# Kernel optimization log

Hardware: AMD Instinct MI355X
Metric: run time of the kernel (lower is better)

## Reference

```python
import jax, jax.numpy as jnp
import numpy as np
import math

NUM_BUCKETS = 32
MAX_DISTANCE = 128
N_HEADS = 16
D_KV = 64


def _relative_position_bucket(relative_position, num_buckets=NUM_BUCKETS, max_distance=MAX_DISTANCE):
    # bidirectional (encoder) variant: is_decoder=False
    nb = num_buckets // 2
    rel_buckets = (relative_position > 0).astype(jnp.int32) * nb
    rp = jnp.abs(relative_position)
    max_exact = nb // 2
    is_small = rp < max_exact
    rp_large = max_exact + (
        jnp.log(rp.astype(jnp.float32) / max_exact)
        / math.log(max_distance / max_exact)
        * (nb - max_exact)
    ).astype(jnp.int32)
    rp_large = jnp.minimum(rp_large, nb - 1)
    return rel_buckets + jnp.where(is_small, rp, rp_large)


def compute_position_bias(rel_bias_table, q_len, k_len):
    ctx = jnp.arange(q_len, dtype=jnp.int32)[:, None]
    mem = jnp.arange(k_len, dtype=jnp.int32)[None, :]
    buckets = _relative_position_bucket(mem - ctx)  # [q_len, k_len]
    values = rel_bias_table[buckets]                # [q_len, k_len, H]
    return jnp.transpose(values, (2, 0, 1))[None]   # [1, H, q_len, k_len]


def setup_inputs() -> dict:
    key = jax.random.key(0)
    ks = jax.random.split(key, 6)
    B, S, D = 2, 2048, 1024
    s = 0.02
    return {
        "hidden_states": jax.random.normal(ks[0], (B, S, D), dtype=jnp.float32),
        "Wq": jax.random.normal(ks[1], (D, N_HEADS * D_KV), dtype=jnp.float32) * s,
        "Wk": jax.random.normal(ks[2], (D, N_HEADS * D_KV), dtype=jnp.float32) * s,
        "Wv": jax.random.normal(ks[3], (D, N_HEADS * D_KV), dtype=jnp.float32) * s,
        "Wo": jax.random.normal(ks[4], (N_HEADS * D_KV, D), dtype=jnp.float32) * s,
        "rel_bias_table": jax.random.normal(ks[5], (NUM_BUCKETS, N_HEADS), dtype=jnp.float32),
    }


def reference(hidden_states, Wq, Wk, Wv, Wo, rel_bias_table):
    B, S, D = hidden_states.shape
    H, dh = N_HEADS, D_KV
    q = (hidden_states @ Wq).reshape(B, S, H, dh)
    k = (hidden_states @ Wk).reshape(B, S, H, dh)
    v = (hidden_states @ Wv).reshape(B, S, H, dh)

    position_bias = compute_position_bias(rel_bias_table, S, S)  # [1,H,S,S]

    scale = 1.0 / math.sqrt(dh)  # applied inside optimized_attention (SDPA convention)
    scores = jnp.einsum('bqhd,bkhd->bhqk', q, k) * scale + position_bias
    probs = jax.nn.softmax(scores, axis=-1)
    ctx = jnp.einsum('bhqk,bkhd->bqhd', probs, v).reshape(B, S, H * dh)
    attn_output = ctx @ Wo
    return attn_output
```

## Files before the change

kernel.cpp:

```cpp
#include <hip/hip_runtime.h>

typedef __attribute__((ext_vector_type(8))) short s16x8;
typedef __attribute__((ext_vector_type(4))) float f32x4;
typedef __attribute__((ext_vector_type(4))) unsigned int u32x4;
typedef __attribute__((ext_vector_type(2))) unsigned int u32x2;
typedef unsigned short u16;
typedef unsigned int u32;

#define LOG2E 1.4426950408889634f

__device__ __forceinline__ u16 f2bf(float x) {
  u32 u = __float_as_uint(x);
  u += 0x7FFFu + ((u >> 16) & 1u);
  return (u16)(u >> 16);
}

__device__ __forceinline__ u32 pack_bf_trunc(float lo, float hi) {
  return (__float_as_uint(lo) >> 16) | (__float_as_uint(hi) & 0xFFFF0000u);
}

__device__ __forceinline__ void gl_lds16(const void* g, void* l) {
  __builtin_amdgcn_global_load_lds((const __attribute__((address_space(1))) void*)g,
                                   (__attribute__((address_space(3))) void*)l, 16, 0, 0);
}

#define MFMA16(a, b, c) __builtin_amdgcn_mfma_f32_16x16x32_bf16((a), (b), (c), 0, 0, 0)


__global__ __launch_bounds__(256) void prep(const float* __restrict__ hs,
                                            const float* __restrict__ Wq,
                                            const float* __restrict__ Wk,
                                            const float* __restrict__ Wv,
                                            const float* __restrict__ Wo,
                                            const float* __restrict__ tbl,
                                            u16* __restrict__ hsb,
                                            u16* __restrict__ wt,
                                            u16* __restrict__ wot,
                                            float* __restrict__ biasT) {
  const int blk = blockIdx.x;
  const int tid = threadIdx.x;
  if (blk < 2048) {
    const int i = blk * 256 + tid;
    const float4* s4 = (const float4*)hs;
    float4 a = s4[i * 2];
    float4 b = s4[i * 2 + 1];
    s16x8 o;
    o[0] = (short)f2bf(a.x); o[1] = (short)f2bf(a.y);
    o[2] = (short)f2bf(a.z); o[3] = (short)f2bf(a.w);
    o[4] = (short)f2bf(b.x); o[5] = (short)f2bf(b.y);
    o[6] = (short)f2bf(b.z); o[7] = (short)f2bf(b.w);
    *(s16x8*)&hsb[i * 8] = o;
  } else if (blk < 4096) {
    int r = blk - 2048;
    const int sel = r >> 9;
    r &= 511;
    const float* W = sel == 0 ? Wq : (sel == 1 ? Wk : (sel == 2 ? Wv : Wo));
    u16* dst = sel == 3 ? wot : wt + sel * 1048576;
    const int n = (r & 15) * 64 + (tid & 63);
    const int kb = (r >> 4) * 32 + (tid >> 6) * 8;
    s16x8 o;
#pragma unroll
    for (int j = 0; j < 8; ++j) o[j] = (short)f2bf(W[(kb + j) * 1024 + n]);
    *(s16x8*)&dst[n * 1024 + kb] = o;
  } else {
    const int i = (blk - 4096) * 256 + tid;
    const int h = i >> 12, dp = i & 4095;
    const int delta = dp - 2047;
    const int rp = delta < 0 ? -delta : delta;
    int bucket = delta > 0 ? 16 : 0;
    if (rp < 8)
      bucket += rp;
    else
      bucket += 8 + (rp >= 12) + (rp >= 16) + (rp >= 23) + (rp >= 32) +
                (rp >= 46) + (rp >= 64) + (rp >= 91);
    biasT[i] = tbl[bucket * 16 + h] * LOG2E;
  }
}

__global__ __launch_bounds__(256) void vtrans(const u16* __restrict__ V,
                                              u16* __restrict__ VT) {
  const int tid = threadIdx.x;
  const int bh = blockIdx.y;
  const int b = bh >> 4, h = bh & 15;
  const int s0 = blockIdx.x * 32;
  const int d = tid & 63;
  const int si = tid >> 6;
  s16x8 o;
#pragma unroll
  for (int j = 0; j < 8; ++j)
    o[j] = (short)V[(b * 2048 + s0 + si * 8 + j) * 1024 + h * 64 + d];
  *(s16x8*)&VT[(bh * 64 + d) * 2048 + s0 + si * 8] = o;
}


__device__ __forceinline__ void gemm_core(const u16* __restrict__ A,
                                          const u16* __restrict__ Bt,
                                          int m0, int n0,
                                          u16* As, u16* Bs, f32x4 acc[4][4]) {
  const int tid = threadIdx.x;
  const int w = tid >> 6, l = tid & 63, g = l >> 4, m15 = l & 15;
  const int wr = (w >> 1) * 64, wc = (w & 1) * 64;
#pragma unroll
  for (int i = 0; i < 4; ++i)
#pragma unroll
    for (int j = 0; j < 4; ++j) acc[i][j] = (f32x4){0.f, 0.f, 0.f, 0.f};

  for (int kt = 0; kt < 16; ++kt) {
    const int k0 = kt * 64;
    __syncthreads();
#pragma unroll
    for (int c = 0; c < 4; ++c) {
      const int idx = c * 256 + tid;
      const int row = idx >> 3, col16 = idx & 7;
      const int scol = col16 ^ (row & 7);
      gl_lds16(&A[(m0 + row) * 1024 + k0 + scol * 8], (char*)As + c * 4096 + w * 1024);
      gl_lds16(&Bt[(n0 + row) * 1024 + k0 + scol * 8], (char*)Bs + c * 4096 + w * 1024);
    }
    __syncthreads();
#pragma unroll
    for (int ks = 0; ks < 2; ++ks) {
      s16x8 af[4], bf[4];
#pragma unroll
      for (int mf = 0; mf < 4; ++mf) {
        const int row = wr + mf * 16 + m15;
        af[mf] = *(const s16x8*)&As[(row * 8 + ((ks * 4 + g) ^ (row & 7))) * 8];
      }
#pragma unroll
      for (int nf = 0; nf < 4; ++nf) {
        const int row = wc + nf * 16 + m15;
        bf[nf] = *(const s16x8*)&Bs[(row * 8 + ((ks * 4 + g) ^ (row & 7))) * 8];
      }
#pragma unroll
      for (int mf = 0; mf < 4; ++mf)
#pragma unroll
        for (int nf = 0; nf < 4; ++nf)
          acc[mf][nf] = MFMA16(af[mf], bf[nf], acc[mf][nf]);
    }
  }
}

__global__ __launch_bounds__(256) void gemm_qkv(const u16* __restrict__ X,
                                                const u16* __restrict__ Wt,
                                                u16* __restrict__ Q,
                                                u16* __restrict__ Kb,
                                                u16* __restrict__ Vb) {
  __shared__ u16 As[8192], Bs[8192];
  f32x4 acc[4][4];
  const int flat = blockIdx.x;
  const int x = flat & 7, i = flat >> 3;
  const int m0 = ((x & 3) * 8 + (i & 7)) * 128;
  const int n0 = ((x >> 2) * 12 + (i >> 3)) * 128;
  gemm_core(X, Wt, m0, n0, As, Bs, acc);

  const int tid = threadIdx.x;
  const int w = tid >> 6, l = tid & 63, g = l >> 4, m15 = l & 15;
  const int wr = (w >> 1) * 64, wc = (w & 1) * 64;
  const int nsel = n0 >> 10;
  u16* dst = nsel == 0 ? Q : (nsel == 1 ? Kb : Vb);
  const float scale = nsel == 0 ? 0.125f * LOG2E : 1.0f;
  const int ncol0 = (n0 & 1023) + wc;
#pragma unroll
  for (int mf = 0; mf < 4; ++mf) {
    const int rbase = m0 + wr + mf * 16 + g * 4;
#pragma unroll
    for (int nf = 0; nf < 4; ++nf) {
      const int col = ncol0 + nf * 16 + m15;
#pragma unroll
      for (int r = 0; r < 4; ++r)
        dst[(rbase + r) * 1024 + col] = f2bf(acc[mf][nf][r] * scale);
    }
  }
}

__global__ __launch_bounds__(256) void gemm_out(const u16* __restrict__ CTX,
                                                const u16* __restrict__ Wot,
                                                float* __restrict__ Out) {
  __shared__ u16 As[8192], Bs[8192];
  f32x4 acc[4][4];
  const int flat = blockIdx.x;
  const int x = flat & 7, i = flat >> 3;
  const int m0 = ((x & 3) * 8 + (i & 7)) * 128;
  const int n0 = ((x >> 2) * 4 + (i >> 3)) * 128;
  gemm_core(CTX, Wot, m0, n0, As, Bs, acc);

  const int tid = threadIdx.x;
  const int w = tid >> 6, l = tid & 63, g = l >> 4, m15 = l & 15;
  const int wr = (w >> 1) * 64, wc = (w & 1) * 64;
#pragma unroll
  for (int mf = 0; mf < 4; ++mf) {
    const int rbase = m0 + wr + mf * 16 + g * 4;
#pragma unroll
    for (int nf = 0; nf < 4; ++nf) {
      const int col = n0 + wc + nf * 16 + m15;
#pragma unroll
      for (int r = 0; r < 4; ++r)
        Out[(rbase + r) * 1024 + col] = acc[mf][nf][r];
    }
  }
}


__global__ __launch_bounds__(256, 2) void attn_kernel(const u16* __restrict__ Qg,
                                                      const u16* __restrict__ Kg,
                                                      const u16* __restrict__ VTg,
                                                      const float* __restrict__ biasT,
                                                      const float* __restrict__ tbl,
                                                      u16* __restrict__ CTX) {
  __shared__ u16 KT[2][4096];
  __shared__ u16 VTs[2][4096];

  const int tid = threadIdx.x;
  const int w = tid >> 6, l = tid & 63, g = l >> 4, m15 = l & 15;
  const int flat = blockIdx.x;
  const int nf_ = (flat & 7) * 64 + (flat >> 3);
  const int qblk = nf_ & 15, bh = nf_ >> 4;
  const int b = bh >> 4, h = bh & 15;
  const int qw = qblk * 128 + w * 32;

  const float fpos = tbl[31 * 16 + h] * LOG2E;
  const float fneg = tbl[15 * 16 + h] * LOG2E;

  s16x8 aq[2][2];
#pragma unroll
  for (int qs = 0; qs < 2; ++qs) {
    const u16* qp = &Qg[(b * 2048 + qw + qs * 16 + m15) * 1024 + h * 64 + g * 8];
    aq[qs][0] = *(const s16x8*)qp;
    aq[qs][1] = *(const s16x8*)(qp + 32);
  }

  s16x8 vone;
#pragma unroll
  for (int j = 0; j < 8; ++j) vone[j] = (short)0x3F80;

  f32x4 o[2][4];
  f32x4 ls4[2];
#pragma unroll
  for (int qs = 0; qs < 2; ++qs) {
    ls4[qs] = (f32x4){0.f, 0.f, 0.f, 0.f};
#pragma unroll
    for (int d = 0; d < 4; ++d) o[qs][d] = (f32x4){0.f, 0.f, 0.f, 0.f};
  }

  const u16* Kbase = &Kg[(b * 2048) * 1024 + h * 64];
  const u16* Vbase = &VTg[bh * 64 * 2048];

#define STAGE(buf, kv0)                                                          \
  {                                                                              \
    _Pragma("unroll") for (int c = 0; c < 2; ++c) {                              \
      const int idx = c * 256 + tid;                                             \
      const int row = idx >> 3, col16 = idx & 7;                                 \
      const int scol = col16 ^ (row & 7);                                        \
      gl_lds16(&Kbase[(kv0 + row) * 1024 + scol * 8],                            \
               (char*)KT + (buf)*8192 + c * 4096 + w * 1024);                    \
      gl_lds16(&Vbase[row * 2048 + (kv0) + scol * 8],                            \
               (char*)VTs + (buf)*8192 + c * 4096 + w * 1024);                   \
    }                                                                            \
  }

  STAGE(0, 0);
  int cur = 0;
  for (int t = 0; t < 32; ++t) {
    const int kv0 = t * 64;
    __syncthreads();
    if (t < 31) STAGE(cur ^ 1, kv0 + 64);

    const u16* KTc = &KT[cur][0];
    const u16* VTc = &VTs[cur][0];

    f32x4 s[2][4];
    const int diff = kv0 - qw;
    if (diff <= -160 || diff >= 128) {
      const float bc = diff > 0 ? fpos : fneg;
#pragma unroll
      for (int qs = 0; qs < 2; ++qs)
#pragma unroll
        for (int c = 0; c < 4; ++c) s[qs][c] = (f32x4){bc, bc, bc, bc};
    } else {
#pragma unroll
      for (int qs = 0; qs < 2; ++qs) {
        const float* bp = &biasT[h * 4096 + kv0 + g * 4 - qw - qs * 16 - m15 + 2047];
#pragma unroll
        for (int c = 0; c < 4; ++c)
#pragma unroll
          for (int r = 0; r < 4; ++r) s[qs][c][r] = bp[c * 16 + r];
      }
    }

#pragma unroll
    for (int ks = 0; ks < 2; ++ks) {
#pragma unroll
      for (int c = 0; c < 4; ++c) {
        const int row = c * 16 + m15;
        const s16x8 bk = *(const s16x8*)&KTc[(row * 8 + ((ks * 4 + g) ^ (row & 7))) * 8];
        s[0][c] = MFMA16(bk, aq[0][ks], s[0][c]);
        s[1][c] = MFMA16(bk, aq[1][ks], s[1][c]);
      }
    }

    s16x8 pa[2][2];
#pragma unroll
    for (int qs = 0; qs < 2; ++qs) {
      u32 w01[4], w23[4];
#pragma unroll
      for (int c = 0; c < 4; ++c) {
        w01[c] = pack_bf_trunc(__builtin_amdgcn_exp2f(s[qs][c][0]),
                               __builtin_amdgcn_exp2f(s[qs][c][1]));
        w23[c] = pack_bf_trunc(__builtin_amdgcn_exp2f(s[qs][c][2]),
                               __builtin_amdgcn_exp2f(s[qs][c][3]));
      }
#pragma unroll
      for (int ks = 0; ks < 2; ++ks) {
        u32x2 rA = __builtin_amdgcn_permlane32_swap(w01[2 * ks], w01[2 * ks + 1], false, false);
        u32x2 rB = __builtin_amdgcn_permlane16_swap(rA[0], rA[1], false, false);
        u32x2 rC = __builtin_amdgcn_permlane32_swap(w23[2 * ks], w23[2 * ks + 1], false, false);
        u32x2 rD = __builtin_amdgcn_permlane16_swap(rC[0], rC[1], false, false);
        const u32x4 pd = (u32x4){rB[0], rD[0], rB[1], rD[1]};
        pa[qs][ks] = __builtin_bit_cast(s16x8, pd);
      }
    }

#pragma unroll
    for (int ks = 0; ks < 2; ++ks) {
#pragma unroll
      for (int d = 0; d < 4; ++d) {
        const int rowv = d * 16 + m15;
        const s16x8 bv = *(const s16x8*)&VTc[(rowv * 8 + ((ks * 4 + g) ^ (rowv & 7))) * 8];
        o[0][d] = MFMA16(pa[0][ks], bv, o[0][d]);
        o[1][d] = MFMA16(pa[1][ks], bv, o[1][d]);
      }
      ls4[0] = MFMA16(pa[0][ks], vone, ls4[0]);
      ls4[1] = MFMA16(pa[1][ks], vone, ls4[1]);
    }
    cur ^= 1;
  }
#undef STAGE

#pragma unroll
  for (int qs = 0; qs < 2; ++qs) {
    f32x4 inv;
#pragma unroll
    for (int r = 0; r < 4; ++r) inv[r] = 1.0f / ls4[qs][r];
    const int orow = b * 2048 + qw + qs * 16 + g * 4;
    const int ocol = h * 64 + m15;
#pragma unroll
    for (int d = 0; d < 4; ++d) {
#pragma unroll
      for (int r = 0; r < 4; ++r)
        CTX[(orow + r) * 1024 + ocol + d * 16] = f2bf(o[qs][d][r] * inv[r]);
    }
  }
}


extern "C" void kernel_launch(void* const* d_in, const int* in_sizes, int n_in,
                              void* d_out, int out_size, void* d_ws, size_t ws_size,
                              hipStream_t stream) {
  (void)in_sizes; (void)n_in; (void)out_size; (void)ws_size;
  const float* hs  = (const float*)d_in[0];
  const float* Wq  = (const float*)d_in[1];
  const float* Wk  = (const float*)d_in[2];
  const float* Wv  = (const float*)d_in[3];
  const float* Wo  = (const float*)d_in[4];
  const float* tbl = (const float*)d_in[5];

  char* ws = (char*)d_ws;
  u16* hsb   = (u16*)(ws);
  u16* wt    = (u16*)(ws + 8388608);
  u16* wot   = (u16*)(ws + 14680064);
  u16* q     = (u16*)(ws + 16777216);
  u16* k     = (u16*)(ws + 25165824);
  u16* v     = (u16*)(ws + 33554432);
  u16* vt    = (u16*)(ws + 41943040);
  u16* ctx   = (u16*)(ws + 50331648);
  float* biasT = (float*)(ws + 58720256);

  prep<<<4352, 256, 0, stream>>>(hs, Wq, Wk, Wv, Wo, tbl, hsb, wt, wot, biasT);
  gemm_qkv<<<768, 256, 0, stream>>>(hsb, wt, q, k, v);
  vtrans<<<dim3(64, 32), 256, 0, stream>>>(v, vt);
  attn_kernel<<<512, 256, 0, stream>>>(q, k, vt, biasT, tbl, ctx);
  gemm_out<<<256, 256, 0, stream>>>(ctx, wot, (float*)d_out);
}
```

Baseline: 125.8 us.

## Split attention KV range in two, fuse V transpose into QKV GEMM, add merge

The attention kernel now splits each head's key range into two halves, launching twice as many blocks with occupancy raised to 4 waves per SIMD, and writes unnormalized partial outputs plus row sums. A new merge kernel adds the two halves and normalizes. Because softmax here has no max subtraction, the partials combine without rescaling. The V transpose kernel is removed: the QKV GEMM epilogue writes V directly in transposed layout. s_setprio brackets are added around the MFMA sections. The cost is an extra merge pass, extra partial-output traffic, and bf16 rounding of the partial sums.

Result: slower. 129.3 us (+2.8%).

```diff
diff --git a/kernel.cpp b/kernel.cpp
--- a/kernel.cpp
+++ b/kernel.cpp
@@ -1,6 +1,7 @@
 #include <hip/hip_runtime.h>
 
 typedef __attribute__((ext_vector_type(8))) short s16x8;
+typedef __attribute__((ext_vector_type(4))) short s16x4;
 typedef __attribute__((ext_vector_type(4))) float f32x4;
 typedef __attribute__((ext_vector_type(4))) unsigned int u32x4;
 typedef __attribute__((ext_vector_type(2))) unsigned int u32x2;
@@ -13,6 +14,10 @@
   u32 u = __float_as_uint(x);
   u += 0x7FFFu + ((u >> 16) & 1u);
   return (u16)(u >> 16);
+}
+
+__device__ __forceinline__ float bf2f(u16 x) {
+  return __uint_as_float((u32)x << 16);
 }
 
 __device__ __forceinline__ u32 pack_bf_trunc(float lo, float hi) {
@@ -77,21 +82,6 @@
   }
 }
 
-__global__ __launch_bounds__(256) void vtrans(const u16* __restrict__ V,
-                                              u16* __restrict__ VT) {
-  const int tid = threadIdx.x;
-  const int bh = blockIdx.y;
-  const int b = bh >> 4, h = bh & 15;
-  const int s0 = blockIdx.x * 32;
-  const int d = tid & 63;
-  const int si = tid >> 6;
-  s16x8 o;
-#pragma unroll
-  for (int j = 0; j < 8; ++j)
-    o[j] = (short)V[(b * 2048 + s0 + si * 8 + j) * 1024 + h * 64 + d];
-  *(s16x8*)&VT[(bh * 64 + d) * 2048 + s0 + si * 8] = o;
-}
-
 
 __device__ __forceinline__ void gemm_core(const u16* __restrict__ A,
                                           const u16* __restrict__ Bt,
@@ -143,7 +133,7 @@
                                                 const u16* __restrict__ Wt,
                                                 u16* __restrict__ Q,
                                                 u16* __restrict__ Kb,
-                                                u16* __restrict__ Vb) {
+                                                u16* __restrict__ VT) {
   __shared__ u16 As[8192], Bs[8192];
   f32x4 acc[4][4];
   const int flat = blockIdx.x;
@@ -156,18 +146,35 @@
   const int w = tid >> 6, l = tid & 63, g = l >> 4, m15 = l & 15;
   const int wr = (w >> 1) * 64, wc = (w & 1) * 64;
   const int nsel = n0 >> 10;
-  u16* dst = nsel == 0 ? Q : (nsel == 1 ? Kb : Vb);
-  const float scale = nsel == 0 ? 0.125f * LOG2E : 1.0f;
   const int ncol0 = (n0 & 1023) + wc;
-#pragma unroll
-  for (int mf = 0; mf < 4; ++mf) {
-    const int rbase = m0 + wr + mf * 16 + g * 4;
-#pragma unroll
-    for (int nf = 0; nf < 4; ++nf) {
-      const int col = ncol0 + nf * 16 + m15;
-#pragma unroll
-      for (int r = 0; r < 4; ++r)
-        dst[(rbase + r) * 1024 + col] = f2bf(acc[mf][nf][r] * scale);
+  if (nsel == 2) {
+#pragma unroll
+    for (int mf = 0; mf < 4; ++mf) {
+      const int rbase = m0 + wr + mf * 16 + g * 4;
+      const int bhb = (rbase >> 11) * 16;
+      const int rloc = rbase & 2047;
+#pragma unroll
+      for (int nf = 0; nf < 4; ++nf) {
+        const int col = ncol0 + nf * 16 + m15;
+        s16x4 pk;
+#pragma unroll
+        for (int r = 0; r < 4; ++r) pk[r] = (short)f2bf(acc[mf][nf][r]);
+        *(s16x4*)&VT[((bhb + (col >> 6)) * 64 + (col & 63)) * 2048 + rloc] = pk;
+      }
+    }
+  } else {
+    u16* dst = nsel == 0 ? Q : Kb;
+    const float scale = nsel == 0 ? 0.125f * LOG2E : 1.0f;
+#pragma unroll
+    for (int mf = 0; mf < 4; ++mf) {
+      const int rbase = m0 + wr + mf * 16 + g * 4;
+#pragma unroll
+      for (int nf = 0; nf < 4; ++nf) {
+        const int col = ncol0 + nf * 16 + m15;
+#pragma unroll
+        for (int r = 0; r < 4; ++r)
+          dst[(rbase + r) * 1024 + col] = f2bf(acc[mf][nf][r] * scale);
+      }
     }
   }
 }
@@ -200,22 +207,30 @@
 }
 
 
-__global__ __launch_bounds__(256, 2) void attn_kernel(const u16* __restrict__ Qg,
+__global__ __launch_bounds__(256, 4) void attn_kernel(const u16* __restrict__ Qg,
                                                       const u16* __restrict__ Kg,
                                                       const u16* __restrict__ VTg,
                                                       const float* __restrict__ biasT,
                                                       const float* __restrict__ tbl,
-                                                      u16* __restrict__ CTX) {
+                                                      u16* __restrict__ po0,
+                                                      u16* __restrict__ po1,
+                                                      float* __restrict__ pls) {
   __shared__ u16 KT[2][4096];
   __shared__ u16 VTs[2][4096];
 
   const int tid = threadIdx.x;
   const int w = tid >> 6, l = tid & 63, g = l >> 4, m15 = l & 15;
   const int flat = blockIdx.x;
-  const int nf_ = (flat & 7) * 64 + (flat >> 3);
-  const int qblk = nf_ & 15, bh = nf_ >> 4;
+  const int nf_ = (flat & 7) * 128 + (flat >> 3);
+  const int bh = nf_ >> 5;
+  const int rem = nf_ & 31;
+  const int half = rem >> 4, qblk = rem & 15;
   const int b = bh >> 4, h = bh & 15;
   const int qw = qblk * 128 + w * 32;
+  const int kvbase = half * 1024;
+
+  u16* poh = half ? po1 : po0;
+  float* plsh = pls + half * 65536;
 
   const float fpos = tbl[31 * 16 + h] * LOG2E;
   const float fneg = tbl[15 * 16 + h] * LOG2E;
@@ -241,8 +256,8 @@
     for (int d = 0; d < 4; ++d) o[qs][d] = (f32x4){0.f, 0.f, 0.f, 0.f};
   }
 
-  const u16* Kbase = &Kg[(b * 2048) * 1024 + h * 64];
-  const u16* Vbase = &VTg[bh * 64 * 2048];
+  const u16* Kbase = &Kg[(b * 2048 + kvbase) * 1024 + h * 64];
+  const u16* Vbase = &VTg[bh * 64 * 2048 + kvbase];
 
 #define STAGE(buf, kv0)                                                          \
   {                                                                              \
@@ -259,16 +274,16 @@
 
   STAGE(0, 0);
   int cur = 0;
-  for (int t = 0; t < 32; ++t) {
+  for (int t = 0; t < 16; ++t) {
     const int kv0 = t * 64;
     __syncthreads();
-    if (t < 31) STAGE(cur ^ 1, kv0 + 64);
+    if (t < 15) STAGE(cur ^ 1, kv0 + 64);
 
     const u16* KTc = &KT[cur][0];
     const u16* VTc = &VTs[cur][0];
 
     f32x4 s[2][4];
-    const int diff = kv0 - qw;
+    const int diff = kvbase + kv0 - qw;
     if (diff <= -160 || diff >= 128) {
       const float bc = diff > 0 ? fpos : fneg;
 #pragma unroll
@@ -278,7 +293,8 @@
     } else {
 #pragma unroll
       for (int qs = 0; qs < 2; ++qs) {
-        const float* bp = &biasT[h * 4096 + kv0 + g * 4 - qw - qs * 16 - m15 + 2047];
+        const float* bp =
+            &biasT[h * 4096 + kvbase + kv0 + g * 4 - qw - qs * 16 - m15 + 2047];
 #pragma unroll
         for (int c = 0; c < 4; ++c)
 #pragma unroll
@@ -286,6 +302,7 @@
       }
     }
 
+    __builtin_amdgcn_s_setprio(1);
 #pragma unroll
     for (int ks = 0; ks < 2; ++ks) {
 #pragma unroll
@@ -296,6 +313,7 @@
         s[1][c] = MFMA16(bk, aq[1][ks], s[1][c]);
       }
     }
+    __builtin_amdgcn_s_setprio(0);
 
     s16x8 pa[2][2];
 #pragma unroll
@@ -319,6 +337,7 @@
       }
     }
 
+    __builtin_amdgcn_s_setprio(1);
 #pragma unroll
     for (int ks = 0; ks < 2; ++ks) {
 #pragma unroll
@@ -331,24 +350,41 @@
       ls4[0] = MFMA16(pa[0][ks], vone, ls4[0]);
       ls4[1] = MFMA16(pa[1][ks], vone, ls4[1]);
     }
+    __builtin_amdgcn_s_setprio(0);
     cur ^= 1;
   }
 #undef STAGE
 
 #pragma unroll
   for (int qs = 0; qs < 2; ++qs) {
-    f32x4 inv;
-#pragma unroll
-    for (int r = 0; r < 4; ++r) inv[r] = 1.0f / ls4[qs][r];
     const int orow = b * 2048 + qw + qs * 16 + g * 4;
     const int ocol = h * 64 + m15;
 #pragma unroll
-    for (int d = 0; d < 4; ++d) {
-#pragma unroll
-      for (int r = 0; r < 4; ++r)
-        CTX[(orow + r) * 1024 + ocol + d * 16] = f2bf(o[qs][d][r] * inv[r]);
-    }
-  }
+    for (int r = 0; r < 4; ++r) {
+#pragma unroll
+      for (int d = 0; d < 4; ++d)
+        poh[(orow + r) * 1024 + ocol + d * 16] = f2bf(o[qs][d][r]);
+      if (m15 == 0) plsh[(orow + r) * 16 + h] = ls4[qs][r];
+    }
+  }
+}
+
+__global__ __launch_bounds__(256) void merge(const u16* __restrict__ po0,
+                                             const u16* __restrict__ po1,
+                                             const float* __restrict__ pls,
+                                             u16* __restrict__ ctx) {
+  const int i = blockIdx.x * 256 + threadIdx.x;
+  const int row = i >> 7;
+  const int seg = i & 127;
+  const int h = seg >> 3;
+  const float den = 1.0f / (pls[row * 16 + h] + pls[65536 + row * 16 + h]);
+  const s16x8 a = *(const s16x8*)&po0[row * 1024 + seg * 8];
+  const s16x8 b = *(const s16x8*)&po1[row * 1024 + seg * 8];
+  s16x8 o;
+#pragma unroll
+  for (int j = 0; j < 8; ++j)
+    o[j] = (short)f2bf((bf2f((u16)a[j]) + bf2f((u16)b[j])) * den);
+  *(s16x8*)&ctx[row * 1024 + seg * 8] = o;
 }
 
 
@@ -369,14 +405,16 @@
   u16* wot   = (u16*)(ws + 14680064);
   u16* q     = (u16*)(ws + 16777216);
   u16* k     = (u16*)(ws + 25165824);
-  u16* v     = (u16*)(ws + 33554432);
+  u16* po0   = (u16*)(ws + 33554432);
   u16* vt    = (u16*)(ws + 41943040);
   u16* ctx   = (u16*)(ws + 50331648);
   float* biasT = (float*)(ws + 58720256);
+  u16* po1   = hsb;
+  float* pls = (float*)wt;
 
   prep<<<4352, 256, 0, stream>>>(hs, Wq, Wk, Wv, Wo, tbl, hsb, wt, wot, biasT);
-  gemm_qkv<<<768, 256, 0, stream>>>(hsb, wt, q, k, v);
-  vtrans<<<dim3(64, 32), 256, 0, stream>>>(v, vt);
-  attn_kernel<<<512, 256, 0, stream>>>(q, k, vt, biasT, tbl, ctx);
+  gemm_qkv<<<768, 256, 0, stream>>>(hsb, wt, q, k, vt);
+  attn_kernel<<<1024, 256, 0, stream>>>(q, k, vt, biasT, tbl, po0, po1, pls);
+  merge<<<2048, 256, 0, stream>>>(po0, po1, pls, ctx);
   gemm_out<<<256, 256, 0, stream>>>(ctx, wot, (float*)d_out);
 }
```
